# Kernel tuning notes

Measured on AMD Instinct MI355X. Metric: run time of the kernel, lower is better.

Reference implementation:

```python
import jax, jax.numpy as jnp
import numpy as np

NUM_TOKENS = 1048576
NUM_EXPERTS = 64


def setup_inputs() -> dict:
    key = jax.random.key(0)
    router_logits_fp32 = jax.random.normal(key, (NUM_TOKENS, NUM_EXPERTS), dtype=jnp.float32)
    return {"router_logits_fp32": router_logits_fp32, "top_k": 8}


def reference(router_logits_fp32, top_k):
    # Fused softmax over experts + top-k selection (aiter.topk_softmax with renorm=True).
    probs = jax.nn.softmax(router_logits_fp32, axis=-1)          # [T, E]
    topk_weights, topk_ids = jax.lax.top_k(probs, top_k)         # [T, K], [T, K]
    # renormalize selected weights to sum to 1 per token (the trailing True flag)
    topk_weights = topk_weights / jnp.sum(topk_weights, axis=-1, keepdims=True)
    num_tokens = router_logits_fp32.shape[0]
    # token_expert_indices[t, k] = t * top_k + k (row-major source-row mapping used
    # later for the token permutation/scatter into expert buffers)
    token_expert_indices = jnp.arange(num_tokens * top_k, dtype=jnp.int32).reshape(num_tokens, top_k)
    return topk_weights, topk_ids.astype(jnp.int32), token_expert_indices
```

## Files before the change

kernel.cpp:

```cpp
#include <hip/hip_runtime.h>
#include <stdint.h>


typedef float f32x4 __attribute__((ext_vector_type(4)));

#define DPP_QUAD_XOR1   0xB1
#define DPP_QUAD_XOR2   0x4E
#define DPP_HALF_MIRROR 0x141

template<int CTRL>
static __device__ __forceinline__ uint32_t dpp32(uint32_t x) {
    return (uint32_t)__builtin_amdgcn_update_dpp(0, (int)x, CTRL, 0xF, 0xF, true);
}
template<int CTRL>
static __device__ __forceinline__ uint64_t dpp64(uint64_t x) {
    int lo = __builtin_amdgcn_update_dpp(0, (int)(uint32_t)x,         CTRL, 0xF, 0xF, true);
    int hi = __builtin_amdgcn_update_dpp(0, (int)(uint32_t)(x >> 32), CTRL, 0xF, 0xF, true);
    return ((uint64_t)(uint32_t)hi << 32) | (uint32_t)lo;
}
template<int CTRL>
static __device__ __forceinline__ float dppf(float x) {
    int i = __builtin_amdgcn_update_dpp(0, __float_as_int(x), CTRL, 0xF, 0xF, true);
    return __int_as_float(i);
}

#define CE32(x, y) { uint32_t gt_ = (x > y) ? x : y; uint32_t lt_ = (x > y) ? y : x; \
                     x = gt_; y = lt_; }
#define CEU(x, y) { uint64_t a_ = x, b_ = y; bool c_ = a_ < b_; \
                    x = c_ ? b_ : a_; y = c_ ? a_ : b_; }

template<int CTRL>
static __device__ __forceinline__ void merge_u32(uint32_t k[8]) {
    uint32_t m[8];
#pragma unroll
    for (int i = 0; i < 8; ++i) {
        uint32_t p = dpp32<CTRL>(k[7 - i]);
        m[i] = (k[i] > p) ? k[i] : p;
    }
    CE32(m[0], m[4]) CE32(m[1], m[5]) CE32(m[2], m[6]) CE32(m[3], m[7])
    CE32(m[0], m[2]) CE32(m[1], m[3]) CE32(m[4], m[6]) CE32(m[5], m[7])
    CE32(m[0], m[1]) CE32(m[2], m[3]) CE32(m[4], m[5]) CE32(m[6], m[7])
#pragma unroll
    for (int i = 0; i < 8; ++i) k[i] = m[i];
}

static __device__ __forceinline__ uint32_t mono(float v) {
    uint32_t u = __float_as_uint(v);
    return u ^ (uint32_t)(((int32_t)u >> 31) | 0x80000000);
}
static __device__ __forceinline__ float unmono(uint32_t m) {
    uint32_t u = (m & 0x80000000u) ? (m ^ 0x80000000u) : ~m;
    return __uint_as_float(u);
}
static __device__ __forceinline__ uint32_t bsel(uint32_t mask, uint32_t b, uint32_t a) {
    return (mask & b) | (~mask & a);
}

__global__ __launch_bounds__(256, 8) void topk_softmax_k(
    const float* __restrict__ logits,
    float* __restrict__ out_w,
    float* __restrict__ out_id,
    float* __restrict__ out_tei,
    int T)
{
    const int  lane = threadIdx.x & 63;
    const int  wv   = (int)(threadIdx.x >> 6);
    const long t0   = (long)blockIdx.x * 32 + (long)wv * 8;
    if (t0 >= T) return;

    const int  sub = lane & 7;
    const bool act = (t0 + (lane >> 3)) < T;

    const f32x4* src = reinterpret_cast<const f32x4*>(logits)
                     + (act ? (t0 * 16 + (long)lane * 2) : 0);
    f32x4 a = __builtin_nontemporal_load(src);
    f32x4 b = __builtin_nontemporal_load(src + 1);

    uint32_t o[8] = { mono(a.x), mono(a.y), mono(a.z), mono(a.w),
                      mono(b.x), mono(b.y), mono(b.z), mono(b.w) };

    const uint32_t cb = (uint32_t)(63 - sub * 8);
    uint32_t k[8];
#pragma unroll
    for (int j = 0; j < 8; ++j)
        k[j] = (o[j] & 0xFFFFFFC0u) | (cb - (uint32_t)j);

    CE32(k[0],k[1]) CE32(k[2],k[3]) CE32(k[4],k[5]) CE32(k[6],k[7])
    CE32(k[0],k[2]) CE32(k[1],k[3]) CE32(k[4],k[6]) CE32(k[5],k[7])
    CE32(k[1],k[2]) CE32(k[5],k[6])
    CE32(k[0],k[4]) CE32(k[1],k[5]) CE32(k[2],k[6]) CE32(k[3],k[7])
    CE32(k[2],k[4]) CE32(k[3],k[5])
    CE32(k[1],k[2]) CE32(k[3],k[4]) CE32(k[5],k[6])

    merge_u32<DPP_QUAD_XOR1>(k);
    merge_u32<DPP_QUAD_XOR2>(k);
    merge_u32<DPP_HALF_MIRROR>(k);

    const uint32_t k7 = k[7];
    uint32_t qcnt = 0;
#pragma unroll
    for (int j = 0; j < 8; ++j)
        qcnt += ((o[j] | 63u) >= k7) ? 1u : 0u;
    qcnt += dpp32<DPP_QUAD_XOR1>(qcnt);
    qcnt += dpp32<DPP_QUAD_XOR2>(qcnt);
    qcnt += dpp32<DPP_HALF_MIRROR>(qcnt);
    uint32_t dmin = 0xFFFFFFFFu;
#pragma unroll
    for (int i = 0; i < 7; ++i) {
        uint32_t d = (k[i] ^ k[i + 1]) >> 6;
        dmin = (d < dmin) ? d : dmin;
    }

    const uint32_t m1 = 0u - (uint32_t)(sub & 1);
    const uint32_t m2 = 0u - (uint32_t)((sub >> 1) & 1);
    const uint32_t m4 = 0u - (uint32_t)((sub >> 2) & 1);
    uint32_t t4a = bsel(m4, k[4], k[0]);
    uint32_t t4b = bsel(m4, k[5], k[1]);
    uint32_t t4c = bsel(m4, k[6], k[2]);
    uint32_t t4d = bsel(m4, k[7], k[3]);
    uint32_t t2a = bsel(m2, t4c, t4a);
    uint32_t t2b = bsel(m2, t4d, t4b);
    uint32_t sel = bsel(m1, t2b, t2a);

    uint32_t selmono = sel  & 0xFFFFFFC0u;
    uint32_t maxmono = k[0] & 0xFFFFFFC0u;
    int      idx     = 63 - (int)(sel & 63u);

    if (__any((qcnt != 8u) || (dmin == 0u))) {
        uint64_t kk[8];
#pragma unroll
        for (int j = 0; j < 8; ++j)
            kk[j] = ((uint64_t)o[j] << 6) | (uint64_t)(cb - (uint32_t)j);

        CEU(kk[0],kk[1]) CEU(kk[2],kk[3]) CEU(kk[4],kk[5]) CEU(kk[6],kk[7])
        CEU(kk[0],kk[2]) CEU(kk[1],kk[3]) CEU(kk[4],kk[6]) CEU(kk[5],kk[7])
        CEU(kk[1],kk[2]) CEU(kk[5],kk[6])
        CEU(kk[0],kk[4]) CEU(kk[1],kk[5]) CEU(kk[2],kk[6]) CEU(kk[3],kk[7])
        CEU(kk[2],kk[4]) CEU(kk[3],kk[5])
        CEU(kk[1],kk[2]) CEU(kk[3],kk[4]) CEU(kk[5],kk[6])

        uint64_t mykey = 0, mtop = 0;
#pragma unroll
        for (int r = 0; r < 8; ++r) {
            uint64_t w = kk[0];
            { uint64_t t = dpp64<DPP_QUAD_XOR1>(w);   if (t > w) w = t; }
            { uint64_t t = dpp64<DPP_QUAD_XOR2>(w);   if (t > w) w = t; }
            { uint64_t t = dpp64<DPP_HALF_MIRROR>(w); if (t > w) w = t; }
            if (r == 0)   mtop  = w;
            if (sub == r) mykey = w;
            bool pop = (kk[0] == w);
            kk[0] = pop ? kk[1] : kk[0];
            kk[1] = pop ? kk[2] : kk[1];
            kk[2] = pop ? kk[3] : kk[2];
            kk[3] = pop ? kk[4] : kk[3];
            kk[4] = pop ? kk[5] : kk[4];
            kk[5] = pop ? kk[6] : kk[5];
            kk[6] = pop ? kk[7] : kk[6];
            kk[7] = pop ? 0     : kk[7];
        }
        selmono = (uint32_t)(mykey >> 6);
        maxmono = (uint32_t)(mtop  >> 6);
        idx = 63 - (int)((uint32_t)mykey & 63u);
    }

    const float v  = unmono(selmono);
    const float mv = unmono(maxmono);
    float e = __expf(v - mv);
    float s = e;
    s += dppf<DPP_QUAD_XOR1>(s);
    s += dppf<DPP_QUAD_XOR2>(s);
    s += dppf<DPP_HALF_MIRROR>(s);
    float wgt = e * __builtin_amdgcn_rcpf(s);

    if (act) {
        const long oi = t0 * 8 + lane;
        __builtin_nontemporal_store(wgt,        &out_w[oi]);
        __builtin_nontemporal_store((float)idx, &out_id[oi]);
        __builtin_nontemporal_store((float)oi,  &out_tei[oi]);
    }
}

extern "C" void kernel_launch(void* const* d_in, const int* in_sizes, int n_in,
                              void* d_out, int out_size, void* d_ws, size_t ws_size,
                              hipStream_t stream) {
    const float* logits = (const float*)d_in[0];
    const int T = in_sizes[0] / 64;

    float* outw = (float*)d_out;
    float* outi = outw + (size_t)T * 8;
    float* outt = outi + (size_t)T * 8;

    const int blocks = (T + 31) / 32;
    hipLaunchKernelGGL(topk_softmax_k, dim3(blocks), dim3(256), 0, stream,
                       logits, outw, outi, outt, T);
}
```

Baseline: 73.43 us.

## Process two token tiles per wave and reload logits in rare fallback path

Each wave now handles 16 tokens as two 8-token tiles, issuing all four vector loads up front so both tiles' memory latency overlaps. This halves the number of blocks. The per-lane monotone keys are no longer kept live through the fast path, which cuts register pressure. The rare exact-tie fallback reloads the logits from global memory instead of keeping them in registers. In exchange there are more registers in flight for the second tile's data and an extra reload whenever the fallback triggers.

```diff
diff --git a/kernel.cpp b/kernel.cpp
--- a/kernel.cpp
+++ b/kernel.cpp
@@ -56,34 +56,24 @@
     return (mask & b) | (~mask & a);
 }
 
-__global__ __launch_bounds__(256, 8) void topk_softmax_k(
-    const float* __restrict__ logits,
-    float* __restrict__ out_w,
-    float* __restrict__ out_id,
-    float* __restrict__ out_tei,
-    int T)
+static __device__ __forceinline__ void process_tile(
+    const f32x4* __restrict__ src,
+    f32x4 a, f32x4 b, int sub,
+    float* __restrict__ out_w, float* __restrict__ out_id,
+    float* __restrict__ out_tei, long oi, bool act)
 {
-    const int  lane = threadIdx.x & 63;
-    const int  wv   = (int)(threadIdx.x >> 6);
-    const long t0   = (long)blockIdx.x * 32 + (long)wv * 8;
-    if (t0 >= T) return;
-
-    const int  sub = lane & 7;
-    const bool act = (t0 + (lane >> 3)) < T;
-
-    const f32x4* src = reinterpret_cast<const f32x4*>(logits)
-                     + (act ? (t0 * 16 + (long)lane * 2) : 0);
-    f32x4 a = __builtin_nontemporal_load(src);
-    f32x4 b = __builtin_nontemporal_load(src + 1);
-
-    uint32_t o[8] = { mono(a.x), mono(a.y), mono(a.z), mono(a.w),
-                      mono(b.x), mono(b.y), mono(b.z), mono(b.w) };
-
     const uint32_t cb = (uint32_t)(63 - sub * 8);
-    uint32_t k[8];
-#pragma unroll
-    for (int j = 0; j < 8; ++j)
-        k[j] = (o[j] & 0xFFFFFFC0u) | (cb - (uint32_t)j);
+
+    uint32_t k[8], q[8];
+    {
+        const float vals[8] = {a.x, a.y, a.z, a.w, b.x, b.y, b.z, b.w};
+#pragma unroll
+        for (int j = 0; j < 8; ++j) {
+            uint32_t m = mono(vals[j]);
+            k[j] = (m & 0xFFFFFFC0u) | (cb - (uint32_t)j);
+            q[j] = m | 63u;
+        }
+    }
 
     CE32(k[0],k[1]) CE32(k[2],k[3]) CE32(k[4],k[5]) CE32(k[6],k[7])
     CE32(k[0],k[2]) CE32(k[1],k[3]) CE32(k[4],k[6]) CE32(k[5],k[7])
@@ -100,7 +90,7 @@
     uint32_t qcnt = 0;
 #pragma unroll
     for (int j = 0; j < 8; ++j)
-        qcnt += ((o[j] | 63u) >= k7) ? 1u : 0u;
+        qcnt += (q[j] >= k7) ? 1u : 0u;
     qcnt += dpp32<DPP_QUAD_XOR1>(qcnt);
     qcnt += dpp32<DPP_QUAD_XOR2>(qcnt);
     qcnt += dpp32<DPP_HALF_MIRROR>(qcnt);
@@ -127,10 +117,13 @@
     int      idx     = 63 - (int)(sel & 63u);
 
     if (__any((qcnt != 8u) || (dmin == 0u))) {
+        f32x4 ra = __builtin_nontemporal_load(src);
+        f32x4 rb = __builtin_nontemporal_load(src + 1);
+        const float rv[8] = {ra.x, ra.y, ra.z, ra.w, rb.x, rb.y, rb.z, rb.w};
         uint64_t kk[8];
 #pragma unroll
         for (int j = 0; j < 8; ++j)
-            kk[j] = ((uint64_t)o[j] << 6) | (uint64_t)(cb - (uint32_t)j);
+            kk[j] = ((uint64_t)mono(rv[j]) << 6) | (uint64_t)(cb - (uint32_t)j);
 
         CEU(kk[0],kk[1]) CEU(kk[2],kk[3]) CEU(kk[4],kk[5]) CEU(kk[6],kk[7])
         CEU(kk[0],kk[2]) CEU(kk[1],kk[3]) CEU(kk[4],kk[6]) CEU(kk[5],kk[7])
@@ -173,11 +166,39 @@
     float wgt = e * __builtin_amdgcn_rcpf(s);
 
     if (act) {
-        const long oi = t0 * 8 + lane;
         __builtin_nontemporal_store(wgt,        &out_w[oi]);
         __builtin_nontemporal_store((float)idx, &out_id[oi]);
         __builtin_nontemporal_store((float)oi,  &out_tei[oi]);
     }
+}
+
+__global__ __launch_bounds__(256, 8) void topk_softmax_k(
+    const float* __restrict__ logits,
+    float* __restrict__ out_w,
+    float* __restrict__ out_id,
+    float* __restrict__ out_tei,
+    int T)
+{
+    const int  lane = threadIdx.x & 63;
+    const int  wv   = (int)(threadIdx.x >> 6);
+    const long t0   = ((long)blockIdx.x * 4 + wv) * 16;
+    if (t0 >= T) return;
+
+    const int  sub  = lane & 7;
+    const bool act0 = (t0 +     (lane >> 3)) < T;
+    const bool act1 = (t0 + 8 + (lane >> 3)) < T;
+
+    const f32x4* base = reinterpret_cast<const f32x4*>(logits);
+    const f32x4* s0 = base + (act0 ? (t0 * 16 + (long)lane * 2)       : 0);
+    const f32x4* s1 = base + (act1 ? ((t0 + 8) * 16 + (long)lane * 2) : 0);
+
+    f32x4 a0 = __builtin_nontemporal_load(s0);
+    f32x4 b0 = __builtin_nontemporal_load(s0 + 1);
+    f32x4 a1 = __builtin_nontemporal_load(s1);
+    f32x4 b1 = __builtin_nontemporal_load(s1 + 1);
+
+    process_tile(s0, a0, b0, sub, out_w, out_id, out_tei, t0 * 8 + lane,        act0);
+    process_tile(s1, a1, b1, sub, out_w, out_id, out_tei, (t0 + 8) * 8 + lane,  act1);
 }
 
 extern "C" void kernel_launch(void* const* d_in, const int* in_sizes, int n_in,
@@ -190,7 +211,8 @@
     float* outi = outw + (size_t)T * 8;
     float* outt = outi + (size_t)T * 8;
 
-    const int blocks = (T + 31) / 32;
-    hipLaunchKernelGGL(topk_softmax_k, dim3(blocks), dim3(256), 0, stream,
+    const long nwaves = ((long)T + 15) / 16;
+    const long blocks = (nwaves + 3) / 4;
+    hipLaunchKernelGGL(topk_softmax_k, dim3((uint32_t)blocks), dim3(256), 0, stream,
                        logits, outw, outi, outt, T);
 }
```

Measured after the change: 73.40 us. Within noise of the previous version (-0.0%).
